# Performance work log

Hardware: AMD Instinct MI355X
Metric: run time of the kernel (lower is better)

Reference implementation:

```python
import jax, jax.numpy as jnp
import numpy as np

D_MODEL = 2048
NUM_HEADS = 16
HEAD_DIM = D_MODEL // NUM_HEADS  # 128
BASE = 10000.0


def rotate_half(x):
    x1, x2 = x[..., : x.shape[-1] // 2], x[..., x.shape[-1] // 2 :]
    return jnp.concatenate((-x2, x1), axis=-1)


def setup_inputs() -> dict:
    key = jax.random.key(0)
    ks = jax.random.split(key, 9)
    B, S, D = 2, 2048, D_MODEL
    s = 1.0 / np.sqrt(D)
    return {
        "x": jax.random.normal(ks[0], (B, S, D), dtype=jnp.float32),
        "Wq": jax.random.normal(ks[1], (D, D), dtype=jnp.float32) * s,
        "bq": jnp.zeros((D,), dtype=jnp.float32),
        "Wk": jax.random.normal(ks[2], (D, D), dtype=jnp.float32) * s,
        "bk": jnp.zeros((D,), dtype=jnp.float32),
        "Wv": jax.random.normal(ks[3], (D, D), dtype=jnp.float32) * s,
        "bv": jnp.zeros((D,), dtype=jnp.float32),
        "Wo": jax.random.normal(ks[4], (D, D), dtype=jnp.float32) * s,
        "bo": jnp.zeros((D,), dtype=jnp.float32),
    }


def reference(x, Wq, bq, Wk, bk, Wv, bv, Wo, bo):
    B, S, D = x.shape
    H, hd = NUM_HEADS, HEAD_DIM

    def proj(W, b):
        # nn.Linear: x @ W^T + b, then split heads -> [B, H, S, hd]
        return (x @ W.T + b).reshape(B, S, H, hd).transpose(0, 2, 1, 3)

    q = proj(Wq, bq)
    k = proj(Wk, bk)
    v = proj(Wv, bv)

    # Rotary embedding table (note: original applies cos()/sin() to a
    # tensor that already contains [sin(si), cos(si)] — reproduced faithfully).
    positions = jnp.arange(S, dtype=jnp.float32)
    inv_freq = 1.0 / (BASE ** (jnp.arange(0, hd, 2, dtype=jnp.float32) / hd))
    sinusoid = positions[:, None] * inv_freq[None, :]            # [S, hd/2]
    emb = jnp.concatenate((jnp.sin(sinusoid), jnp.cos(sinusoid)), axis=-1)  # [S, hd]
    cos_e = jnp.cos(emb)  # broadcast over [B, H, S, hd]
    sin_e = jnp.sin(emb)

    q_rot = q * cos_e + rotate_half(q) * sin_e
    k_rot = k * cos_e + rotate_half(k) * sin_e

    scale = 1.0 / jnp.sqrt(jnp.asarray(hd, dtype=x.dtype))
    attn = jnp.einsum("bhqd,bhkd->bhqk", q_rot, k_rot) * scale
    attn = jax.nn.softmax(attn, axis=-1)
    out = jnp.einsum("bhqk,bhkd->bhqd", attn, v)
    out = out.transpose(0, 2, 1, 3).reshape(B, S, D)
    return out @ Wo.T + bo
```

## Files before the change

kernel.cpp:

```cpp
#include <hip/hip_runtime.h>
#include <math.h>

#define D_MODEL 2048
#define NHEADS  16
#define HD      128
#define SEQ     2048
#define BATCH   2
#define SCALE   0.08838834764831845f
#define SMAX    20.0f

typedef __attribute__((ext_vector_type(8))) short short8;
typedef __attribute__((ext_vector_type(4))) float f32x4;

#define MFMA16(a,b,c) __builtin_amdgcn_mfma_f32_16x16x32_bf16((a),(b),(c),0,0,0)

__device__ __forceinline__ unsigned short f2bf(float x){
    unsigned u = __float_as_uint(x);
    return (unsigned short)((u + 0x7FFFu + ((u>>16)&1u)) >> 16);
}
__device__ __forceinline__ float bf2f(unsigned short h){ return __uint_as_float(((unsigned)h)<<16); }

__device__ __forceinline__ void async16(void* lds, const void* g){
    __builtin_amdgcn_global_load_lds((const __attribute__((address_space(1))) unsigned int*)g,
                                     (__attribute__((address_space(3))) unsigned int*)lds, 16, 0, 0);
}

__device__ __forceinline__ void split4(float4 v, ushort4* h, ushort4* l){
    h->x=f2bf(v.x); l->x=f2bf(v.x-bf2f(h->x));
    h->y=f2bf(v.y); l->y=f2bf(v.y-bf2f(h->y));
    h->z=f2bf(v.z); l->z=f2bf(v.z-bf2f(h->z));
    h->w=f2bf(v.w); l->w=f2bf(v.w-bf2f(h->w));
}

__global__ __launch_bounds__(256)
void prep_all(const float* __restrict__ x, const float* __restrict__ Wq,
              const float* __restrict__ Wk, const float* __restrict__ Wv,
              unsigned short* __restrict__ Xhi, unsigned short* __restrict__ Xlo,
              unsigned short* __restrict__ WqHi, unsigned short* __restrict__ WqLo,
              unsigned short* __restrict__ WkHi, unsigned short* __restrict__ WkLo,
              unsigned short* __restrict__ WvHi,
              float4* __restrict__ tab)
{
    const int b = blockIdx.x, t = threadIdx.x;
    if (b < 8192) {
        int i = b*256 + t;
        ushort4 h,l; split4(((const float4*)x)[i], &h, &l);
        ((ushort4*)Xhi)[i]=h; ((ushort4*)Xlo)[i]=l;
    } else if (b < 12288) {
        int i = (b-8192)*256 + t;
        ushort4 h,l; split4(((const float4*)Wq)[i], &h, &l);
        ((ushort4*)WqHi)[i]=h; ((ushort4*)WqLo)[i]=l;
    } else if (b < 16384) {
        int i = (b-12288)*256 + t;
        ushort4 h,l; split4(((const float4*)Wk)[i], &h, &l);
        ((ushort4*)WkHi)[i]=h; ((ushort4*)WkLo)[i]=l;
    } else if (b < 20480) {
        int i = (b-16384)*256 + t;
        ushort4 h,l; split4(((const float4*)Wv)[i], &h, &l);
        ((ushort4*)WvHi)[i]=h;
    } else {
        int i = (b-20480)*256 + t;
        int s = i >> 6, d = i & 63;
        float f = powf(10000.0f, -(float)d * (1.0f/64.0f));
        float sv = (float)s * f;
        float sn = sinf(sv), cs = cosf(sv);
        tab[i] = (float4){cosf(sn), sinf(sn), cosf(cs), sinf(cs)};
    }
}

__global__ __launch_bounds__(256)
void split_w(const float* __restrict__ src, unsigned short* __restrict__ hi,
             unsigned short* __restrict__ lo, int n4)
{
    int i = blockIdx.x*256 + threadIdx.x;
    if (i >= n4) return;
    ushort4 h,l; split4(((const float4*)src)[i], &h, &l);
    ((ushort4*)hi)[i]=h; ((ushort4*)lo)[i]=l;
}

template<bool THREE, int Q>
__device__ __forceinline__ void col_mfma(const short8 (&ah)[4], const short8 (&al)[4],
                                         const short8 (&bh)[4], const short8 (&bl)[4],
                                         f32x4 (&acc)[4][4])
{
    __builtin_amdgcn_s_setprio(1);
    acc[0][Q] = MFMA16(ah[0], bh[Q], acc[0][Q]);
    acc[1][Q] = MFMA16(ah[1], bh[Q], acc[1][Q]);
    acc[2][Q] = MFMA16(ah[2], bh[Q], acc[2][Q]);
    acc[3][Q] = MFMA16(ah[3], bh[Q], acc[3][Q]);
    acc[0][Q] = MFMA16(al[0], bh[Q], acc[0][Q]);
    acc[1][Q] = MFMA16(al[1], bh[Q], acc[1][Q]);
    acc[2][Q] = MFMA16(al[2], bh[Q], acc[2][Q]);
    acc[3][Q] = MFMA16(al[3], bh[Q], acc[3][Q]);
    if constexpr (THREE) {
        acc[0][Q] = MFMA16(ah[0], bl[Q], acc[0][Q]);
        acc[1][Q] = MFMA16(ah[1], bl[Q], acc[1][Q]);
        acc[2][Q] = MFMA16(ah[2], bl[Q], acc[2][Q]);
        acc[3][Q] = MFMA16(ah[3], bl[Q], acc[3][Q]);
    }
    __builtin_amdgcn_s_setprio(0);
}

template<bool THREE>
__device__ __forceinline__ void gemm_core(const unsigned short* __restrict__ Agh,
                                          const unsigned short* __restrict__ Agl,
                                          const unsigned short* __restrict__ Bgh,
                                          const unsigned short* __restrict__ Bgl,
                                          unsigned short* lds, int m0, int n0,
                                          f32x4 (&acc)[4][4])
{
    const int t = threadIdx.x, w = t>>6, lane = t&63;
    const int quad = lane>>4, l15 = lane&15;
    const int wm = w>>1, wn = w&1;

    unsigned short *c0 = lds, *c1 = lds + 24576, *c2 = lds + 49152;

    auto stageA = [&](unsigned short* P, const unsigned short* SRC, int u, int kt2){
        int idx = t + u*512; int rw = idx>>2, sg = idx&3;
        int sgp = sg ^ ((rw>>1)&3);
        async16((char*)(P + rw*32 + sg*8), SRC + (size_t)(m0+rw)*2048 + kt2 + sgp*8);
    };
    auto stageB = [&](unsigned short* P, const unsigned short* SRC, int kt2){
        int rw = t>>2, sg = t&3; int sgp = sg ^ ((rw>>1)&3);
        async16((char*)(P + rw*32 + sg*8), SRC + (size_t)(n0+rw)*2048 + kt2 + sgp*8);
    };

    stageA(c0,        Agh, 0, 0);  stageA(c0,        Agh, 1, 0);
    stageA(c0+8192,   Agl, 0, 0);  stageA(c0+8192,   Agl, 1, 0);
    stageB(c0+16384,  Bgh, 0);
    if constexpr (THREE) stageB(c0+20480, Bgl, 0);
    stageA(c1,        Agh, 0, 32); stageA(c1,        Agh, 1, 32);
    stageA(c1+8192,   Agl, 0, 32); stageA(c1+8192,   Agl, 1, 32);
    stageB(c1+16384,  Bgh, 32);
    if constexpr (THREE) stageB(c1+20480, Bgl, 32);

    for (int kt = 0; kt < 64; ++kt) {
        if (kt == 63) {
            asm volatile("s_waitcnt vmcnt(0)" ::: "memory");
        } else if constexpr (THREE) {
            asm volatile("s_waitcnt vmcnt(6)" ::: "memory");
        } else {
            asm volatile("s_waitcnt vmcnt(5)" ::: "memory");
        }
        __builtin_amdgcn_s_barrier();
        __builtin_amdgcn_sched_barrier(0);

        const unsigned short* Ah = c0;
        const unsigned short* Al = c0 + 8192;
        const unsigned short* Bh = c0 + 16384;
        const unsigned short* Bl = c0 + 20480;
        const int  kt2 = (kt+2)*32;
        const bool st  = (kt < 62);

        short8 ah[4], al[4], bh[4], bl[4];
#pragma unroll
        for (int mi=0;mi<4;mi++){
            int m = wm*64 + mi*16 + l15;
            int c = (quad ^ ((m>>1)&3))*8;
            ah[mi] = *(const short8*)&Ah[m*32 + c];
            al[mi] = *(const short8*)&Al[m*32 + c];
        }
#pragma unroll
        for (int ni=0;ni<4;ni++){
            int n = wn*64 + ni*16 + l15;
            int c = (quad ^ ((n>>1)&3))*8;
            bh[ni] = *(const short8*)&Bh[n*32 + c];
            if constexpr (THREE) bl[ni] = *(const short8*)&Bl[n*32 + c];
            else                 bl[ni] = (short8){};
        }

        if (st){ stageA(c2,       Agh, 0, kt2); stageA(c2,       Agh, 1, kt2); }
        col_mfma<THREE,0>(ah, al, bh, bl, acc);
        if (st){ stageA(c2+8192,  Agl, 0, kt2); stageA(c2+8192,  Agl, 1, kt2); }
        col_mfma<THREE,1>(ah, al, bh, bl, acc);
        if (st){ stageB(c2+16384, Bgh, kt2); }
        col_mfma<THREE,2>(ah, al, bh, bl, acc);
        if constexpr (THREE) { if (st) stageB(c2+20480, Bgl, kt2); }
        col_mfma<THREE,3>(ah, al, bh, bl, acc);

        unsigned short* tmp = c0; c0 = c1; c1 = c2; c2 = tmp;
    }
}

__global__ __launch_bounds__(512,2)
void gemm_qk(const unsigned short* __restrict__ Xhi_g, const unsigned short* __restrict__ Xlo_g,
             const unsigned short* __restrict__ wsplit,
             const float* __restrict__ bq, const float* __restrict__ bk,
             const float4* __restrict__ tab,
             unsigned short* __restrict__ Qhi, unsigned short* __restrict__ Qlo,
             unsigned short* __restrict__ Khi, unsigned short* __restrict__ Klo)
{
    extern __shared__ unsigned short ldsm[];
    const int z = blockIdx.z;
    const unsigned short* Whi = wsplit + (size_t)z*8388608u;
    const unsigned short* Wlo = Whi + 4194304u;
    const int t = threadIdx.x, w = t>>6, lane = t&63;
    const int quad = lane>>4, l15 = lane&15;
    const int wm = w>>1, wn = w&1;
    const int m0 = blockIdx.y*256, n0 = blockIdx.x*128;

    f32x4 acc[4][4];
#pragma unroll
    for (int i=0;i<4;i++)
#pragma unroll
        for (int j=0;j<4;j++) acc[i][j] = (f32x4){0.f,0.f,0.f,0.f};

    gemm_core<true>(Xhi_g, Xlo_g, Whi, Wlo, ldsm, m0, n0, acc);
    __syncthreads();

    const float* bias = (z==0)?bq:bk;
#pragma unroll
    for (int ni=0;ni<4;ni++){
        float bv_ = bias[n0 + wn*64 + ni*16 + l15];
#pragma unroll
        for (int mi=0;mi<4;mi++){
            acc[mi][ni][0]+=bv_; acc[mi][ni][1]+=bv_; acc[mi][ni][2]+=bv_; acc[mi][ni][3]+=bv_;
        }
    }

    float* xch = (float*)ldsm;
    unsigned short* OHi = (z==0)?Qhi:Khi;
    unsigned short* OLo = (z==0)?Qlo:Klo;
    const float scl = (z==0)?SCALE:1.0f;
    const int h = blockIdx.x;
    const int b = m0>>11;
    const size_t bhbase = ((size_t)(b*16+h)*2048);

    if (wn == 0) {
#pragma unroll
        for (int mi=0;mi<4;mi++)
#pragma unroll
        for (int ni=2;ni<4;ni++)
#pragma unroll
        for (int r=0;r<4;r++)
            xch[(wm*64+mi*16+quad*4+r)*68 + (ni-2)*16+l15] = acc[mi][ni][r];
    } else {
#pragma unroll
        for (int mi=0;mi<4;mi++)
#pragma unroll
        for (int ni=0;ni<2;ni++)
#pragma unroll
        for (int r=0;r<4;r++)
            xch[(wm*64+mi*16+quad*4+r)*68 + 32 + ni*16+l15] = acc[mi][ni][r];
    }
    __syncthreads();

    if (wn == 0) {
#pragma unroll
        for (int ni2=0;ni2<2;ni2++){
            int d = ni2*16 + l15;
#pragma unroll
            for (int mi=0;mi<4;mi++)
#pragma unroll
            for (int r=0;r<4;r++){
                int ml = wm*64 + mi*16 + quad*4 + r;
                int s = (m0 + ml) & 2047;
                float4 tv = tab[s*64 + d];
                float c_lo = acc[mi][ni2][r];
                float c_hi = xch[ml*68 + 32 + d];
                float o1 = (c_lo*tv.x - c_hi*tv.y)*scl;
                float o2 = (c_hi*tv.z + c_lo*tv.w)*scl;
                size_t base = (bhbase + s)*128;
                unsigned short h1=f2bf(o1); OHi[base+d]=h1;    OLo[base+d]=f2bf(o1-bf2f(h1));
                unsigned short h2=f2bf(o2); OHi[base+64+d]=h2; OLo[base+64+d]=f2bf(o2-bf2f(h2));
            }
        }
    } else {
#pragma unroll
        for (int ni2=0;ni2<2;ni2++){
            int d = 32 + ni2*16 + l15;
#pragma unroll
            for (int mi=0;mi<4;mi++)
#pragma unroll
            for (int r=0;r<4;r++){
                int ml = wm*64 + mi*16 + quad*4 + r;
                int s = (m0 + ml) & 2047;
                float4 tv = tab[s*64 + d];
                float c_lo = xch[ml*68 + (d-32)];
                float c_hi = acc[mi][ni2+2][r];
                float o1 = (c_lo*tv.x - c_hi*tv.y)*scl;
                float o2 = (c_hi*tv.z + c_lo*tv.w)*scl;
                size_t base = (bhbase + s)*128;
                unsigned short h1=f2bf(o1); OHi[base+d]=h1;    OLo[base+d]=f2bf(o1-bf2f(h1));
                unsigned short h2=f2bf(o2); OHi[base+64+d]=h2; OLo[base+64+d]=f2bf(o2-bf2f(h2));
            }
        }
    }
}

__global__ __launch_bounds__(512,2)
void gemm_v(const unsigned short* __restrict__ Xhi_g, const unsigned short* __restrict__ Xlo_g,
            const unsigned short* __restrict__ WvHi,
            const float* __restrict__ bv, unsigned short* __restrict__ Vt)
{
    extern __shared__ unsigned short ldsm[];
    const int t = threadIdx.x, w = t>>6, lane = t&63;
    const int quad = lane>>4, l15 = lane&15;
    const int wm = w>>1, wn = w&1;
    const int m0 = blockIdx.y*256, n0 = blockIdx.x*128;

    f32x4 acc[4][4];
#pragma unroll
    for (int i=0;i<4;i++)
#pragma unroll
        for (int j=0;j<4;j++) acc[i][j] = (f32x4){0.f,0.f,0.f,0.f};

    gemm_core<false>(Xhi_g, Xlo_g, WvHi, nullptr, ldsm, m0, n0, acc);
    __syncthreads();

#pragma unroll
    for (int ni=0;ni<4;ni++){
        float bv_ = bv[n0 + wn*64 + ni*16 + l15];
#pragma unroll
        for (int mi=0;mi<4;mi++){
            acc[mi][ni][0]+=bv_; acc[mi][ni][1]+=bv_; acc[mi][ni][2]+=bv_; acc[mi][ni][3]+=bv_;
        }
    }

    unsigned short* vb = ldsm;
#pragma unroll
    for (int mi=0;mi<4;mi++)
#pragma unroll
    for (int ni=0;ni<4;ni++)
#pragma unroll
    for (int r=0;r<4;r++){
        int d  = wn*64 + ni*16 + l15;
        int ml = wm*64 + mi*16 + quad*4 + r;
        vb[d*264 + ml] = f2bf(acc[mi][ni][r]);
    }
    __syncthreads();

    const int b = m0>>11, s0 = m0&2047, h = blockIdx.x;
    unsigned short* vdst = Vt + (size_t)(b*16+h)*128*2048;
    const int dr = t>>2, part = (t&3)*64;
#pragma unroll
    for (int j=0;j<8;j++){
        uint4 v = *(const uint4*)&vb[dr*264 + part + j*8];
        *(uint4*)(vdst + (size_t)dr*2048 + s0 + part + j*8) = v;
    }
}

__global__ __launch_bounds__(512,2)
void gemm_o(const unsigned short* __restrict__ Ahi_g, const unsigned short* __restrict__ Alo_g,
            const unsigned short* __restrict__ Whi_g, const unsigned short* __restrict__ Wlo_g,
            const float* __restrict__ bias, float* __restrict__ out)
{
    extern __shared__ unsigned short ldsm[];
    const int t = threadIdx.x, w = t>>6, lane = t&63;
    const int quad = lane>>4, l15 = lane&15;
    const int wm = w>>1, wn = w&1;
    const int m0 = blockIdx.y*256, n0 = blockIdx.x*128;

    f32x4 acc[4][4];
#pragma unroll
    for (int i=0;i<4;i++)
#pragma unroll
        for (int j=0;j<4;j++) acc[i][j] = (f32x4){0.f,0.f,0.f,0.f};

    gemm_core<true>(Ahi_g, Alo_g, Whi_g, Wlo_g, ldsm, m0, n0, acc);

#pragma unroll
    for (int ni=0;ni<4;ni++){
        int n = n0 + wn*64 + ni*16 + l15;
        float bv_ = bias[n];
#pragma unroll
        for (int mi=0;mi<4;mi++)
#pragma unroll
        for (int r=0;r<4;r++){
            int m = m0 + wm*64 + mi*16 + quad*4 + r;
            out[(size_t)m*2048 + n] = acc[mi][ni][r] + bv_;
        }
    }
}

__global__ __launch_bounds__(256,2)
void flash_mfma(const unsigned short* __restrict__ Qhi, const unsigned short* __restrict__ Qlo,
                const unsigned short* __restrict__ Khi, const unsigned short* __restrict__ Klo,
                const unsigned short* __restrict__ Vt,
                unsigned short* __restrict__ Ohi, unsigned short* __restrict__ Olo)
{
    const int t=threadIdx.x, w=t>>6, lane=t&63, quad=lane>>4, l15=lane&15;
    const int bh = blockIdx.y, qt = blockIdx.x;

    __shared__ __align__(16) unsigned short sm[32768];
    unsigned short* Ps = sm + 24576 + w*2048;

    short8 qf[2][2][4];
    const size_t qrow = (size_t)bh*2048 + qt*128 + w*32;
#pragma unroll
    for (int mb=0;mb<2;mb++){
        size_t r = qrow + mb*16 + l15;
#pragma unroll
        for (int kc=0;kc<4;kc++){
            qf[0][mb][kc] = *(const short8*)(Qhi + r*128 + kc*32 + quad*8);
            qf[1][mb][kc] = *(const short8*)(Qlo + r*128 + kc*32 + quad*8);
        }
    }

    f32x4 O[2][8];
#pragma unroll
    for (int mb=0;mb<2;mb++)
#pragma unroll
        for (int nb=0;nb<8;nb++) O[mb][nb]=(f32x4){0.f,0.f,0.f,0.f};
    float lrow[2][4];
#pragma unroll
    for (int mb=0;mb<2;mb++)
#pragma unroll
        for (int r=0;r<4;r++) lrow[mb][r]=0.f;

    const char* KhiB = (const char*)(Khi + (size_t)bh*2048*128);
    const char* KloB = (const char*)(Klo + (size_t)bh*2048*128);
    const unsigned short* VtB = Vt + (size_t)bh*128*2048;
    char* smb = (char*)sm;

    for (int kt=0; kt<2048; kt+=64) {
#pragma unroll
        for (int i=0;i<4;i++){
            int o16 = t + 256*i;
            int krow = o16>>4, kc = o16&15;
            int kcp = kc ^ (krow&15);
            async16(smb + i*4096 + t*16,         KhiB + (size_t)kt*256 + krow*256 + kcp*16);
            async16(smb + 16384 + i*4096 + t*16, KloB + (size_t)kt*256 + krow*256 + kcp*16);
            int d = (t>>3) + i*32, c = t&7;
            int cp = c ^ (d&7);
            async16(smb + 32768 + i*4096 + t*16, VtB + (size_t)d*2048 + kt + cp*8);
        }
        __syncthreads();

        f32x4 S[2][4];
#pragma unroll
        for (int mb=0;mb<2;mb++)
#pragma unroll
            for (int nb=0;nb<4;nb++) S[mb][nb]=(f32x4){0.f,0.f,0.f,0.f};
#pragma unroll
        for (int kc=0;kc<4;kc++)
#pragma unroll
        for (int nb=0;nb<4;nb++){
            int m = nb*16+l15;
            int c = ((kc*4+quad) ^ (m&15))*8;
            short8 kh = *(const short8*)&sm[m*128 + c];
            short8 kl = *(const short8*)&sm[8192 + m*128 + c];
#pragma unroll
            for (int mb=0;mb<2;mb++){
                S[mb][nb] = MFMA16(qf[0][mb][kc], kh, S[mb][nb]);
                S[mb][nb] = MFMA16(qf[1][mb][kc], kh, S[mb][nb]);
                S[mb][nb] = MFMA16(qf[0][mb][kc], kl, S[mb][nb]);
            }
        }

#pragma unroll
        for (int mb=0;mb<2;mb++)
#pragma unroll
        for (int nb=0;nb<4;nb++)
#pragma unroll
        for (int r=0;r<4;r++){
            float p = __expf(S[mb][nb][r] - SMAX);
            lrow[mb][r] += p;
            int q = mb*16 + quad*4 + r;
            int c = nb*16 + l15;
            Ps[q*64 + (((c>>3)^(q&7))<<3) + (c&7)] = f2bf(p);
        }

#pragma unroll
        for (int kc2=0;kc2<2;kc2++){
            short8 pf0 = *(const short8*)&Ps[(l15)*64      + (((kc2*4+quad)^(l15&7))<<3)];
            short8 pf1 = *(const short8*)&Ps[(16+l15)*64   + (((kc2*4+quad)^(l15&7))<<3)];
#pragma unroll
            for (int nb=0;nb<8;nb++){
                int d = nb*16+l15;
                int c = ((kc2*4+quad) ^ (d&7))*8;
                short8 vf = *(const short8*)&sm[16384 + d*64 + c];
                O[0][nb] = MFMA16(pf0, vf, O[0][nb]);
                O[1][nb] = MFMA16(pf1, vf, O[1][nb]);
            }
        }
        __syncthreads();
    }

#pragma unroll
    for (int mb=0;mb<2;mb++)
#pragma unroll
        for (int d=1;d<16;d<<=1)
#pragma unroll
            for (int r=0;r<4;r++) lrow[mb][r] += __shfl_xor(lrow[mb][r], d);

    const int b = bh>>4, h = bh&15;
#pragma unroll
    for (int mb=0;mb<2;mb++)
#pragma unroll
    for (int nb=0;nb<8;nb++)
#pragma unroll
    for (int r=0;r<4;r++){
        float v = O[mb][nb][r] / lrow[mb][r];
        int qg = qt*128 + w*32 + mb*16 + quad*4 + r;
        size_t base = ((size_t)(b*2048 + qg))*2048 + h*128 + nb*16 + l15;
        unsigned short hh = f2bf(v);
        Ohi[base]=hh; Olo[base]=f2bf(v-bf2f(hh));
    }
}

extern "C" void kernel_launch(void* const* d_in, const int* in_sizes, int n_in,
                              void* d_out, int out_size, void* d_ws, size_t ws_size,
                              hipStream_t stream)
{
    (void)in_sizes; (void)n_in; (void)out_size; (void)ws_size;
    const float* x  = (const float*)d_in[0];
    const float* Wq = (const float*)d_in[1];
    const float* bq = (const float*)d_in[2];
    const float* Wk = (const float*)d_in[3];
    const float* bk = (const float*)d_in[4];
    const float* Wv = (const float*)d_in[5];
    const float* bv = (const float*)d_in[6];
    const float* Wo = (const float*)d_in[7];
    const float* bo = (const float*)d_in[8];
    float* out = (float*)d_out;

    unsigned short* wsB = (unsigned short*)d_ws;
    unsigned short* C0  = wsB + 20971520u;
    unsigned short* Qhi = C0;
    unsigned short* Qlo = C0 + 8388608u;
    unsigned short* Khi = C0 + 16777216u;
    unsigned short* Klo = C0 + 25165824u;
    unsigned short* Vt  = C0 + 33554432u;
    float4* tab = (float4*)(wsB + 62914560u);

    unsigned short* Xhi = (unsigned short*)d_out;
    unsigned short* Xlo = Xhi + 8388608u;

    static bool attr_done = false;
    if (!attr_done) {
        (void)hipFuncSetAttribute(reinterpret_cast<const void*>(&gemm_qk),
                                  hipFuncAttributeMaxDynamicSharedMemorySize, 147456);
        (void)hipFuncSetAttribute(reinterpret_cast<const void*>(&gemm_v),
                                  hipFuncAttributeMaxDynamicSharedMemorySize, 147456);
        (void)hipFuncSetAttribute(reinterpret_cast<const void*>(&gemm_o),
                                  hipFuncAttributeMaxDynamicSharedMemorySize, 147456);
        attr_done = true;
    }

    prep_all<<<20992,256,0,stream>>>(x, Wq, Wk, Wv,
                                     Xhi, Xlo,
                                     wsB,            wsB+4194304u,
                                     wsB+8388608u,   wsB+12582912u,
                                     wsB+16777216u,  tab);

    gemm_qk<<<dim3(16,16,2),512,147456,stream>>>(Xhi, Xlo, wsB, bq, bk, tab,
                                                 Qhi, Qlo, Khi, Klo);
    gemm_v <<<dim3(16,16),  512,147456,stream>>>(Xhi, Xlo, wsB+16777216u, bv, Vt);

    unsigned short* Ohi = wsB;
    unsigned short* Olo = wsB + 8388608u;
    flash_mfma<<<dim3(16,32),256,0,stream>>>(Qhi,Qlo,Khi,Klo,Vt, Ohi, Olo);

    unsigned short* WoHi = C0;
    unsigned short* WoLo = C0 + 4194304u;
    split_w<<<4096,256,0,stream>>>(Wo, WoHi, WoLo, 1048576);

    gemm_o<<<dim3(16,16),512,147456,stream>>>(Ohi, Olo, WoHi, WoLo, bo, out);
}
```

Before: 674.6 us.

## Software-pipeline LDS fragment reads across MFMA column groups in GEMM core

```diff
diff --git a/kernel.cpp b/kernel.cpp
--- a/kernel.cpp
+++ b/kernel.cpp
@@ -78,25 +78,49 @@
     ((ushort4*)hi)[i]=h; ((ushort4*)lo)[i]=l;
 }
 
+template<bool THREE>
+__device__ __forceinline__ void read_A(const unsigned short* Ah, const unsigned short* Al,
+                                       short8 (&ah)[4], short8 (&al)[4],
+                                       int wm, int quad, int l15)
+{
+#pragma unroll
+    for (int mi=0;mi<4;mi++){
+        int m = wm*64 + mi*16 + l15;
+        int c = (quad ^ ((m>>1)&3))*8;
+        ah[mi] = *(const short8*)&Ah[m*32 + c];
+        al[mi] = *(const short8*)&Al[m*32 + c];
+    }
+}
+
+template<bool THREE, int Q>
+__device__ __forceinline__ void read_B(const unsigned short* Bh, const unsigned short* Bl,
+                                       short8& bh, short8& bl, int wn, int quad, int l15)
+{
+    int n = wn*64 + Q*16 + l15;
+    int c = (quad ^ ((n>>1)&3))*8;
+    bh = *(const short8*)&Bh[n*32 + c];
+    if constexpr (THREE) bl = *(const short8*)&Bl[n*32 + c];
+    else                 bl = (short8){};
+}
+
 template<bool THREE, int Q>
 __device__ __forceinline__ void col_mfma(const short8 (&ah)[4], const short8 (&al)[4],
-                                         const short8 (&bh)[4], const short8 (&bl)[4],
-                                         f32x4 (&acc)[4][4])
+                                         short8 bh, short8 bl, f32x4 (&acc)[4][4])
 {
     __builtin_amdgcn_s_setprio(1);
-    acc[0][Q] = MFMA16(ah[0], bh[Q], acc[0][Q]);
-    acc[1][Q] = MFMA16(ah[1], bh[Q], acc[1][Q]);
-    acc[2][Q] = MFMA16(ah[2], bh[Q], acc[2][Q]);
-    acc[3][Q] = MFMA16(ah[3], bh[Q], acc[3][Q]);
-    acc[0][Q] = MFMA16(al[0], bh[Q], acc[0][Q]);
-    acc[1][Q] = MFMA16(al[1], bh[Q], acc[1][Q]);
-    acc[2][Q] = MFMA16(al[2], bh[Q], acc[2][Q]);
-    acc[3][Q] = MFMA16(al[3], bh[Q], acc[3][Q]);
+    acc[0][Q] = MFMA16(ah[0], bh, acc[0][Q]);
+    acc[1][Q] = MFMA16(ah[1], bh, acc[1][Q]);
+    acc[2][Q] = MFMA16(ah[2], bh, acc[2][Q]);
+    acc[3][Q] = MFMA16(ah[3], bh, acc[3][Q]);
+    acc[0][Q] = MFMA16(al[0], bh, acc[0][Q]);
+    acc[1][Q] = MFMA16(al[1], bh, acc[1][Q]);
+    acc[2][Q] = MFMA16(al[2], bh, acc[2][Q]);
+    acc[3][Q] = MFMA16(al[3], bh, acc[3][Q]);
     if constexpr (THREE) {
-        acc[0][Q] = MFMA16(ah[0], bl[Q], acc[0][Q]);
-        acc[1][Q] = MFMA16(ah[1], bl[Q], acc[1][Q]);
-        acc[2][Q] = MFMA16(ah[2], bl[Q], acc[2][Q]);
-        acc[3][Q] = MFMA16(ah[3], bl[Q], acc[3][Q]);
+        acc[0][Q] = MFMA16(ah[0], bl, acc[0][Q]);
+        acc[1][Q] = MFMA16(ah[1], bl, acc[1][Q]);
+        acc[2][Q] = MFMA16(ah[2], bl, acc[2][Q]);
+        acc[3][Q] = MFMA16(ah[3], bl, acc[3][Q]);
     }
     __builtin_amdgcn_s_setprio(0);
 }
@@ -124,61 +148,67 @@
         int rw = t>>2, sg = t&3; int sgp = sg ^ ((rw>>1)&3);
         async16((char*)(P + rw*32 + sg*8), SRC + (size_t)(n0+rw)*2048 + kt2 + sgp*8);
     };
-
-    stageA(c0,        Agh, 0, 0);  stageA(c0,        Agh, 1, 0);
-    stageA(c0+8192,   Agl, 0, 0);  stageA(c0+8192,   Agl, 1, 0);
-    stageB(c0+16384,  Bgh, 0);
-    if constexpr (THREE) stageB(c0+20480, Bgl, 0);
-    stageA(c1,        Agh, 0, 32); stageA(c1,        Agh, 1, 32);
-    stageA(c1+8192,   Agl, 0, 32); stageA(c1+8192,   Agl, 1, 32);
-    stageB(c1+16384,  Bgh, 32);
-    if constexpr (THREE) stageB(c1+20480, Bgl, 32);
+    auto stage_tile = [&](unsigned short* P, int kt2){
+        stageA(P,        Agh, 0, kt2);  stageA(P,        Agh, 1, kt2);
+        stageA(P+8192,   Agl, 0, kt2);  stageA(P+8192,   Agl, 1, kt2);
+        stageB(P+16384,  Bgh, kt2);
+        if constexpr (THREE) stageB(P+20480, Bgl, kt2);
+    };
+
+    stage_tile(c0, 0);
+    stage_tile(c1, 32);
+    if constexpr (THREE) asm volatile("s_waitcnt vmcnt(6)" ::: "memory");
+    else                 asm volatile("s_waitcnt vmcnt(5)" ::: "memory");
+    __builtin_amdgcn_s_barrier();
+    __builtin_amdgcn_sched_barrier(0);
+
+    short8 ah[4], al[4], ahp[4], alp[4];
+    short8 b0h, b0l, b1h, b1l, b2h, b2l, b3h, b3l, b0hp, b0lp;
+    read_A<THREE>(c0, c0+8192, ah, al, wm, quad, l15);
+    read_B<THREE,0>(c0+16384, c0+20480, b0h, b0l, wn, quad, l15);
 
     for (int kt = 0; kt < 64; ++kt) {
-        if (kt == 63) {
-            asm volatile("s_waitcnt vmcnt(0)" ::: "memory");
-        } else if constexpr (THREE) {
-            asm volatile("s_waitcnt vmcnt(6)" ::: "memory");
+        const bool st  = (kt < 62);
+        const int  kt2 = (kt+2)*32;
+
+        read_B<THREE,1>(c0+16384, c0+20480, b1h, b1l, wn, quad, l15);
+        if (st){ stageA(c2,       Agh, 0, kt2); stageA(c2,       Agh, 1, kt2); }
+        col_mfma<THREE,0>(ah, al, b0h, b0l, acc);
+        __builtin_amdgcn_sched_barrier(0);
+
+        read_B<THREE,2>(c0+16384, c0+20480, b2h, b2l, wn, quad, l15);
+        if (st){ stageA(c2+8192,  Agl, 0, kt2); stageA(c2+8192,  Agl, 1, kt2); }
+        col_mfma<THREE,1>(ah, al, b1h, b1l, acc);
+        __builtin_amdgcn_sched_barrier(0);
+
+        read_B<THREE,3>(c0+16384, c0+20480, b3h, b3l, wn, quad, l15);
+        if (st){ stageB(c2+16384, Bgh, kt2); }
+        col_mfma<THREE,2>(ah, al, b2h, b2l, acc);
+        __builtin_amdgcn_sched_barrier(0);
+
+        if constexpr (THREE) { if (st) stageB(c2+20480, Bgl, kt2); }
+        if (kt < 63) {
+            __builtin_amdgcn_sched_barrier(0);
+            asm volatile("s_waitcnt lgkmcnt(0)" ::: "memory");
+            if (st) {
+                if constexpr (THREE) asm volatile("s_waitcnt vmcnt(6)" ::: "memory");
+                else                 asm volatile("s_waitcnt vmcnt(5)" ::: "memory");
+            } else {
+                asm volatile("s_waitcnt vmcnt(0)" ::: "memory");
+            }
+            __builtin_amdgcn_s_barrier();
+            __builtin_amdgcn_sched_barrier(0);
+            read_A<THREE>(c1, c1+8192, ahp, alp, wm, quad, l15);
+            read_B<THREE,0>(c1+16384, c1+20480, b0hp, b0lp, wn, quad, l15);
+            __builtin_amdgcn_sched_barrier(0);
+            col_mfma<THREE,3>(ah, al, b3h, b3l, acc);
+#pragma unroll
+            for (int i=0;i<4;i++){ ah[i]=ahp[i]; al[i]=alp[i]; }
+            b0h = b0hp; b0l = b0lp;
+            unsigned short* tmp = c0; c0 = c1; c1 = c2; c2 = tmp;
         } else {
-            asm volatile("s_waitcnt vmcnt(5)" ::: "memory");
-        }
-        __builtin_amdgcn_s_barrier();
-        __builtin_amdgcn_sched_barrier(0);
-
-        const unsigned short* Ah = c0;
-        const unsigned short* Al = c0 + 8192;
-        const unsigned short* Bh = c0 + 16384;
-        const unsigned short* Bl = c0 + 20480;
-        const int  kt2 = (kt+2)*32;
-        const bool st  = (kt < 62);
-
-        short8 ah[4], al[4], bh[4], bl[4];
-#pragma unroll
-        for (int mi=0;mi<4;mi++){
-            int m = wm*64 + mi*16 + l15;
-            int c = (quad ^ ((m>>1)&3))*8;
-            ah[mi] = *(const short8*)&Ah[m*32 + c];
-            al[mi] = *(const short8*)&Al[m*32 + c];
-        }
-#pragma unroll
-        for (int ni=0;ni<4;ni++){
-            int n = wn*64 + ni*16 + l15;
-            int c = (quad ^ ((n>>1)&3))*8;
-            bh[ni] = *(const short8*)&Bh[n*32 + c];
-            if constexpr (THREE) bl[ni] = *(const short8*)&Bl[n*32 + c];
-            else                 bl[ni] = (short8){};
-        }
-
-        if (st){ stageA(c2,       Agh, 0, kt2); stageA(c2,       Agh, 1, kt2); }
-        col_mfma<THREE,0>(ah, al, bh, bl, acc);
-        if (st){ stageA(c2+8192,  Agl, 0, kt2); stageA(c2+8192,  Agl, 1, kt2); }
-        col_mfma<THREE,1>(ah, al, bh, bl, acc);
-        if (st){ stageB(c2+16384, Bgh, kt2); }
-        col_mfma<THREE,2>(ah, al, bh, bl, acc);
-        if constexpr (THREE) { if (st) stageB(c2+20480, Bgl, kt2); }
-        col_mfma<THREE,3>(ah, al, bh, bl, acc);
-
-        unsigned short* tmp = c0; c0 = c1; c1 = c2; c2 = tmp;
+            col_mfma<THREE,3>(ah, al, b3h, b3l, acc);
+        }
     }
 }
 
```

Result: faster. 635.8 us (-5.8%).

## Use 16-wave GEMM blocks with double-buffered LDS and smaller per-wave tiles

Applied to the files above, without the earlier changes.

```diff
diff --git a/kernel.cpp b/kernel.cpp
--- a/kernel.cpp
+++ b/kernel.cpp
@@ -78,81 +78,55 @@
     ((ushort4*)hi)[i]=h; ((ushort4*)lo)[i]=l;
 }
 
-template<bool THREE, int Q>
-__device__ __forceinline__ void col_mfma(const short8 (&ah)[4], const short8 (&al)[4],
-                                         const short8 (&bh)[4], const short8 (&bl)[4],
-                                         f32x4 (&acc)[4][4])
-{
-    __builtin_amdgcn_s_setprio(1);
-    acc[0][Q] = MFMA16(ah[0], bh[Q], acc[0][Q]);
-    acc[1][Q] = MFMA16(ah[1], bh[Q], acc[1][Q]);
-    acc[2][Q] = MFMA16(ah[2], bh[Q], acc[2][Q]);
-    acc[3][Q] = MFMA16(ah[3], bh[Q], acc[3][Q]);
-    acc[0][Q] = MFMA16(al[0], bh[Q], acc[0][Q]);
-    acc[1][Q] = MFMA16(al[1], bh[Q], acc[1][Q]);
-    acc[2][Q] = MFMA16(al[2], bh[Q], acc[2][Q]);
-    acc[3][Q] = MFMA16(al[3], bh[Q], acc[3][Q]);
-    if constexpr (THREE) {
-        acc[0][Q] = MFMA16(ah[0], bl[Q], acc[0][Q]);
-        acc[1][Q] = MFMA16(ah[1], bl[Q], acc[1][Q]);
-        acc[2][Q] = MFMA16(ah[2], bl[Q], acc[2][Q]);
-        acc[3][Q] = MFMA16(ah[3], bl[Q], acc[3][Q]);
-    }
-    __builtin_amdgcn_s_setprio(0);
-}
-
 template<bool THREE>
 __device__ __forceinline__ void gemm_core(const unsigned short* __restrict__ Agh,
                                           const unsigned short* __restrict__ Agl,
                                           const unsigned short* __restrict__ Bgh,
                                           const unsigned short* __restrict__ Bgl,
                                           unsigned short* lds, int m0, int n0,
-                                          f32x4 (&acc)[4][4])
+                                          f32x4 (&acc)[4][2])
 {
     const int t = threadIdx.x, w = t>>6, lane = t&63;
     const int quad = lane>>4, l15 = lane&15;
-    const int wm = w>>1, wn = w&1;
-
-    unsigned short *c0 = lds, *c1 = lds + 24576, *c2 = lds + 49152;
-
-    auto stageA = [&](unsigned short* P, const unsigned short* SRC, int u, int kt2){
-        int idx = t + u*512; int rw = idx>>2, sg = idx&3;
+    const int wm = w>>2, wn = w&3;
+    constexpr int BUFS = THREE ? 24576 : 20480;
+
+    unsigned short *c0 = lds, *c1 = lds + BUFS;
+
+    auto stageA = [&](unsigned short* P, const unsigned short* SRC, int kt2){
+        int rw = t>>2, sg = t&3;
         int sgp = sg ^ ((rw>>1)&3);
         async16((char*)(P + rw*32 + sg*8), SRC + (size_t)(m0+rw)*2048 + kt2 + sgp*8);
     };
     auto stageB = [&](unsigned short* P, const unsigned short* SRC, int kt2){
-        int rw = t>>2, sg = t&3; int sgp = sg ^ ((rw>>1)&3);
-        async16((char*)(P + rw*32 + sg*8), SRC + (size_t)(n0+rw)*2048 + kt2 + sgp*8);
+        if (t < 512) {
+            int rw = t>>2, sg = t&3;
+            int sgp = sg ^ ((rw>>1)&3);
+            async16((char*)(P + rw*32 + sg*8), SRC + (size_t)(n0+rw)*2048 + kt2 + sgp*8);
+        }
     };
-
-    stageA(c0,        Agh, 0, 0);  stageA(c0,        Agh, 1, 0);
-    stageA(c0+8192,   Agl, 0, 0);  stageA(c0+8192,   Agl, 1, 0);
-    stageB(c0+16384,  Bgh, 0);
-    if constexpr (THREE) stageB(c0+20480, Bgl, 0);
-    stageA(c1,        Agh, 0, 32); stageA(c1,        Agh, 1, 32);
-    stageA(c1+8192,   Agl, 0, 32); stageA(c1+8192,   Agl, 1, 32);
-    stageB(c1+16384,  Bgh, 32);
-    if constexpr (THREE) stageB(c1+20480, Bgl, 32);
+    auto stage_tile = [&](unsigned short* P, int kt2){
+        stageA(P,       Agh, kt2);
+        stageA(P+8192,  Agl, kt2);
+        stageB(P+16384, Bgh, kt2);
+        if constexpr (THREE) stageB(P+20480, Bgl, kt2);
+    };
+
+    stage_tile(c0, 0);
 
     for (int kt = 0; kt < 64; ++kt) {
-        if (kt == 63) {
-            asm volatile("s_waitcnt vmcnt(0)" ::: "memory");
-        } else if constexpr (THREE) {
-            asm volatile("s_waitcnt vmcnt(6)" ::: "memory");
-        } else {
-            asm volatile("s_waitcnt vmcnt(5)" ::: "memory");
-        }
+        asm volatile("s_waitcnt vmcnt(0)" ::: "memory");
         __builtin_amdgcn_s_barrier();
         __builtin_amdgcn_sched_barrier(0);
+
+        if (kt < 63) stage_tile(c1, (kt+1)*32);
 
         const unsigned short* Ah = c0;
         const unsigned short* Al = c0 + 8192;
         const unsigned short* Bh = c0 + 16384;
         const unsigned short* Bl = c0 + 20480;
-        const int  kt2 = (kt+2)*32;
-        const bool st  = (kt < 62);
-
-        short8 ah[4], al[4], bh[4], bl[4];
+
+        short8 ah[4], al[4], bh[2], bl[2];
 #pragma unroll
         for (int mi=0;mi<4;mi++){
             int m = wm*64 + mi*16 + l15;
@@ -161,28 +135,36 @@
             al[mi] = *(const short8*)&Al[m*32 + c];
         }
 #pragma unroll
-        for (int ni=0;ni<4;ni++){
-            int n = wn*64 + ni*16 + l15;
+        for (int ni=0;ni<2;ni++){
+            int n = wn*32 + ni*16 + l15;
             int c = (quad ^ ((n>>1)&3))*8;
             bh[ni] = *(const short8*)&Bh[n*32 + c];
             if constexpr (THREE) bl[ni] = *(const short8*)&Bl[n*32 + c];
             else                 bl[ni] = (short8){};
         }
 
-        if (st){ stageA(c2,       Agh, 0, kt2); stageA(c2,       Agh, 1, kt2); }
-        col_mfma<THREE,0>(ah, al, bh, bl, acc);
-        if (st){ stageA(c2+8192,  Agl, 0, kt2); stageA(c2+8192,  Agl, 1, kt2); }
-        col_mfma<THREE,1>(ah, al, bh, bl, acc);
-        if (st){ stageB(c2+16384, Bgh, kt2); }
-        col_mfma<THREE,2>(ah, al, bh, bl, acc);
-        if constexpr (THREE) { if (st) stageB(c2+20480, Bgl, kt2); }
-        col_mfma<THREE,3>(ah, al, bh, bl, acc);
-
-        unsigned short* tmp = c0; c0 = c1; c1 = c2; c2 = tmp;
-    }
-}
-
-__global__ __launch_bounds__(512,2)
+        __builtin_amdgcn_s_setprio(1);
+#pragma unroll
+        for (int ni=0;ni<2;ni++){
+#pragma unroll
+            for (int mi=0;mi<4;mi++) acc[mi][ni] = MFMA16(ah[mi], bh[ni], acc[mi][ni]);
+#pragma unroll
+            for (int mi=0;mi<4;mi++) acc[mi][ni] = MFMA16(al[mi], bh[ni], acc[mi][ni]);
+            if constexpr (THREE) {
+#pragma unroll
+                for (int mi=0;mi<4;mi++) acc[mi][ni] = MFMA16(ah[mi], bl[ni], acc[mi][ni]);
+            }
+        }
+        __builtin_amdgcn_s_setprio(0);
+
+        asm volatile("s_waitcnt lgkmcnt(0)" ::: "memory");
+        __builtin_amdgcn_sched_barrier(0);
+
+        unsigned short* tmp = c0; c0 = c1; c1 = tmp;
+    }
+}
+
+__global__ __launch_bounds__(1024,4)
 void gemm_qk(const unsigned short* __restrict__ Xhi_g, const unsigned short* __restrict__ Xlo_g,
              const unsigned short* __restrict__ wsplit,
              const float* __restrict__ bq, const float* __restrict__ bk,
@@ -196,22 +178,22 @@
     const unsigned short* Wlo = Whi + 4194304u;
     const int t = threadIdx.x, w = t>>6, lane = t&63;
     const int quad = lane>>4, l15 = lane&15;
-    const int wm = w>>1, wn = w&1;
+    const int wm = w>>2, wn = w&3;
     const int m0 = blockIdx.y*256, n0 = blockIdx.x*128;
 
-    f32x4 acc[4][4];
+    f32x4 acc[4][2];
 #pragma unroll
     for (int i=0;i<4;i++)
 #pragma unroll
-        for (int j=0;j<4;j++) acc[i][j] = (f32x4){0.f,0.f,0.f,0.f};
+        for (int j=0;j<2;j++) acc[i][j] = (f32x4){0.f,0.f,0.f,0.f};
 
     gemm_core<true>(Xhi_g, Xlo_g, Whi, Wlo, ldsm, m0, n0, acc);
     __syncthreads();
 
     const float* bias = (z==0)?bq:bk;
 #pragma unroll
-    for (int ni=0;ni<4;ni++){
-        float bv_ = bias[n0 + wn*64 + ni*16 + l15];
+    for (int ni=0;ni<2;ni++){
+        float bv_ = bias[n0 + wn*32 + ni*16 + l15];
 #pragma unroll
         for (int mi=0;mi<4;mi++){
             acc[mi][ni][0]+=bv_; acc[mi][ni][1]+=bv_; acc[mi][ni][2]+=bv_; acc[mi][ni][3]+=bv_;
@@ -226,38 +208,35 @@
     const int b = m0>>11;
     const size_t bhbase = ((size_t)(b*16+h)*2048);
 
-    if (wn == 0) {
+    const bool loHalf = (wn < 2);
+    const bool loRows = (wm < 2);
+
+    if (loHalf != loRows) {
 #pragma unroll
         for (int mi=0;mi<4;mi++)
 #pragma unroll
-        for (int ni=2;ni<4;ni++)
+        for (int ni=0;ni<2;ni++)
 #pragma unroll
         for (int r=0;r<4;r++)
-            xch[(wm*64+mi*16+quad*4+r)*68 + (ni-2)*16+l15] = acc[mi][ni][r];
-    } else {
-#pragma unroll
-        for (int mi=0;mi<4;mi++)
-#pragma unroll
-        for (int ni=0;ni<2;ni++)
-#pragma unroll
-        for (int r=0;r<4;r++)
-            xch[(wm*64+mi*16+quad*4+r)*68 + 32 + ni*16+l15] = acc[mi][ni][r];
+            xch[(wm*64+mi*16+quad*4+r)*68 + (wn&1)*32 + ni*16 + l15] = acc[mi][ni][r];
     }
     __syncthreads();
 
-    if (wn == 0) {
-#pragma unroll
-        for (int ni2=0;ni2<2;ni2++){
-            int d = ni2*16 + l15;
+    if (loHalf == loRows) {
+#pragma unroll
+        for (int ni=0;ni<2;ni++){
 #pragma unroll
             for (int mi=0;mi<4;mi++)
 #pragma unroll
             for (int r=0;r<4;r++){
-                int ml = wm*64 + mi*16 + quad*4 + r;
-                int s = (m0 + ml) & 2047;
+                int row = wm*64 + mi*16 + quad*4 + r;
+                int d   = (wn&1)*32 + ni*16 + l15;
+                int s   = (m0 + row) & 2047;
                 float4 tv = tab[s*64 + d];
-                float c_lo = acc[mi][ni2][r];
-                float c_hi = xch[ml*68 + 32 + d];
+                float c_own = acc[mi][ni][r];
+                float c_oth = xch[row*68 + d];
+                float c_lo = loRows ? c_own : c_oth;
+                float c_hi = loRows ? c_oth : c_own;
                 float o1 = (c_lo*tv.x - c_hi*tv.y)*scl;
                 float o2 = (c_hi*tv.z + c_lo*tv.w)*scl;
                 size_t base = (bhbase + s)*128;
@@ -265,30 +244,10 @@
                 unsigned short h2=f2bf(o2); OHi[base+64+d]=h2; OLo[base+64+d]=f2bf(o2-bf2f(h2));
             }
         }
-    } else {
-#pragma unroll
-        for (int ni2=0;ni2<2;ni2++){
-            int d = 32 + ni2*16 + l15;
-#pragma unroll
-            for (int mi=0;mi<4;mi++)
-#pragma unroll
-            for (int r=0;r<4;r++){
-                int ml = wm*64 + mi*16 + quad*4 + r;
-                int s = (m0 + ml) & 2047;
-                float4 tv = tab[s*64 + d];
-                float c_lo = xch[ml*68 + (d-32)];
-                float c_hi = acc[mi][ni2+2][r];
-                float o1 = (c_lo*tv.x - c_hi*tv.y)*scl;
-                float o2 = (c_hi*tv.z + c_lo*tv.w)*scl;
-                size_t base = (bhbase + s)*128;
-                unsigned short h1=f2bf(o1); OHi[base+d]=h1;    OLo[base+d]=f2bf(o1-bf2f(h1));
-                unsigned short h2=f2bf(o2); OHi[base+64+d]=h2; OLo[base+64+d]=f2bf(o2-bf2f(h2));
-            }
-        }
-    }
-}
-
-__global__ __launch_bounds__(512,2)
+    }
+}
+
+__global__ __launch_bounds__(1024,4)
 void gemm_v(const unsigned short* __restrict__ Xhi_g, const unsigned short* __restrict__ Xlo_g,
             const unsigned short* __restrict__ WvHi,
             const float* __restrict__ bv, unsigned short* __restrict__ Vt)
@@ -296,21 +255,21 @@
     extern __shared__ unsigned short ldsm[];
     const int t = threadIdx.x, w = t>>6, lane = t&63;
     const int quad = lane>>4, l15 = lane&15;
-    const int wm = w>>1, wn = w&1;
+    const int wm = w>>2, wn = w&3;
     const int m0 = blockIdx.y*256, n0 = blockIdx.x*128;
 
-    f32x4 acc[4][4];
+    f32x4 acc[4][2];
 #pragma unroll
     for (int i=0;i<4;i++)
 #pragma unroll
-        for (int j=0;j<4;j++) acc[i][j] = (f32x4){0.f,0.f,0.f,0.f};
+        for (int j=0;j<2;j++) acc[i][j] = (f32x4){0.f,0.f,0.f,0.f};
 
     gemm_core<false>(Xhi_g, Xlo_g, WvHi, nullptr, ldsm, m0, n0, acc);
     __syncthreads();
 
 #pragma unroll
-    for (int ni=0;ni<4;ni++){
-        float bv_ = bv[n0 + wn*64 + ni*16 + l15];
+    for (int ni=0;ni<2;ni++){
+        float bv_ = bv[n0 + wn*32 + ni*16 + l15];
 #pragma unroll
         for (int mi=0;mi<4;mi++){
             acc[mi][ni][0]+=bv_; acc[mi][ni][1]+=bv_; acc[mi][ni][2]+=bv_; acc[mi][ni][3]+=bv_;
@@ -321,10 +280,10 @@
 #pragma unroll
     for (int mi=0;mi<4;mi++)
 #pragma unroll
-    for (int ni=0;ni<4;ni++)
+    for (int ni=0;ni<2;ni++)
 #pragma unroll
     for (int r=0;r<4;r++){
-        int d  = wn*64 + ni*16 + l15;
+        int d  = wn*32 + ni*16 + l15;
         int ml = wm*64 + mi*16 + quad*4 + r;
         vb[d*264 + ml] = f2bf(acc[mi][ni][r]);
     }
@@ -332,15 +291,15 @@
 
     const int b = m0>>11, s0 = m0&2047, h = blockIdx.x;
     unsigned short* vdst = Vt + (size_t)(b*16+h)*128*2048;
-    const int dr = t>>2, part = (t&3)*64;
-#pragma unroll
-    for (int j=0;j<8;j++){
+    const int dr = t>>3, part = (t&7)*32;
+#pragma unroll
+    for (int j=0;j<4;j++){
         uint4 v = *(const uint4*)&vb[dr*264 + part + j*8];
         *(uint4*)(vdst + (size_t)dr*2048 + s0 + part + j*8) = v;
     }
 }
 
-__global__ __launch_bounds__(512,2)
+__global__ __launch_bounds__(1024,4)
 void gemm_o(const unsigned short* __restrict__ Ahi_g, const unsigned short* __restrict__ Alo_g,
             const unsigned short* __restrict__ Whi_g, const unsigned short* __restrict__ Wlo_g,
             const float* __restrict__ bias, float* __restrict__ out)
@@ -348,20 +307,20 @@
     extern __shared__ unsigned short ldsm[];
     const int t = threadIdx.x, w = t>>6, lane = t&63;
     const int quad = lane>>4, l15 = lane&15;
-    const int wm = w>>1, wn = w&1;
+    const int wm = w>>2, wn = w&3;
     const int m0 = blockIdx.y*256, n0 = blockIdx.x*128;
 
-    f32x4 acc[4][4];
+    f32x4 acc[4][2];
 #pragma unroll
     for (int i=0;i<4;i++)
 #pragma unroll
-        for (int j=0;j<4;j++) acc[i][j] = (f32x4){0.f,0.f,0.f,0.f};
+        for (int j=0;j<2;j++) acc[i][j] = (f32x4){0.f,0.f,0.f,0.f};
 
     gemm_core<true>(Ahi_g, Alo_g, Whi_g, Wlo_g, ldsm, m0, n0, acc);
 
 #pragma unroll
-    for (int ni=0;ni<4;ni++){
-        int n = n0 + wn*64 + ni*16 + l15;
+    for (int ni=0;ni<2;ni++){
+        int n = n0 + wn*32 + ni*16 + l15;
         float bv_ = bias[n];
 #pragma unroll
         for (int mi=0;mi<4;mi++)
@@ -530,11 +489,11 @@
     static bool attr_done = false;
     if (!attr_done) {
         (void)hipFuncSetAttribute(reinterpret_cast<const void*>(&gemm_qk),
-                                  hipFuncAttributeMaxDynamicSharedMemorySize, 147456);
+                                  hipFuncAttributeMaxDynamicSharedMemorySize, 98304);
         (void)hipFuncSetAttribute(reinterpret_cast<const void*>(&gemm_v),
-                                  hipFuncAttributeMaxDynamicSharedMemorySize, 147456);
+                                  hipFuncAttributeMaxDynamicSharedMemorySize, 81920);
         (void)hipFuncSetAttribute(reinterpret_cast<const void*>(&gemm_o),
-                                  hipFuncAttributeMaxDynamicSharedMemorySize, 147456);
+                                  hipFuncAttributeMaxDynamicSharedMemorySize, 98304);
         attr_done = true;
     }
 
@@ -544,9 +503,9 @@
                                      wsB+8388608u,   wsB+12582912u,
                                      wsB+16777216u,  tab);
 
-    gemm_qk<<<dim3(16,16,2),512,147456,stream>>>(Xhi, Xlo, wsB, bq, bk, tab,
+    gemm_qk<<<dim3(16,16,2),1024,98304,stream>>>(Xhi, Xlo, wsB, bq, bk, tab,
                                                  Qhi, Qlo, Khi, Klo);
-    gemm_v <<<dim3(16,16),  512,147456,stream>>>(Xhi, Xlo, wsB+16777216u, bv, Vt);
+    gemm_v <<<dim3(16,16),  1024,81920,stream>>>(Xhi, Xlo, wsB+16777216u, bv, Vt);
 
     unsigned short* Ohi = wsB;
     unsigned short* Olo = wsB + 8388608u;
@@ -556,5 +515,5 @@
     unsigned short* WoLo = C0 + 4194304u;
     split_w<<<4096,256,0,stream>>>(Wo, WoHi, WoLo, 1048576);
 
-    gemm_o<<<dim3(16,16),512,147456,stream>>>(Ohi, Olo, WoHi, WoLo, bo, out);
-}
+    gemm_o<<<dim3(16,16),1024,98304,stream>>>(Ohi, Olo, WoHi, WoLo, bo, out);
+}
```

New measurement: 663.7 us. No clear change (-1.6%).
